# Performance work log

Measured on AMD Instinct MI355X. Metric: run time of the kernel, lower is better.

## Reference

```python
import jax, jax.numpy as jnp
import numpy as np

T, B, D, H, Q = 512, 256, 128, 256, 8


def _qgate(z, params):
    # Exact closed form of the PennyLane circuit:
    #   RX(z_w); RX(params_w) per wire; CNOT chain + wraparound CNOT(n-1,0); <Z_0>
    # => <Z_0> = prod_{w=1..Q-1} cos(z_w + params_w)   (wire 0 cancels out)
    theta = z + params  # (B, Q)
    return jnp.prod(jnp.cos(theta[:, 1:]), axis=1, keepdims=True)  # (B, 1)


def setup_inputs() -> dict:
    key = jax.random.key(0)
    ks = jax.random.split(key, 16)
    inputs = jax.random.normal(ks[0], (T, B, D), dtype=jnp.float32)
    hx0 = jnp.zeros((B, H), dtype=jnp.float32)
    cx0 = jnp.zeros((B, H), dtype=jnp.float32)
    s = 1.0 / np.sqrt(D + H)
    def lin(k1, k2):
        W = jax.random.uniform(k1, (Q, D + H), jnp.float32, -s, s)
        b = jax.random.uniform(k2, (Q,), jnp.float32, -s, s)
        return W, b
    Wf, bf = lin(ks[1], ks[2]); pf = jax.random.normal(ks[3], (Q,), jnp.float32)
    Wi, bi = lin(ks[4], ks[5]); pi = jax.random.normal(ks[6], (Q,), jnp.float32)
    Wu, bu = lin(ks[7], ks[8]); pu = jax.random.normal(ks[9], (Q,), jnp.float32)
    Wo, bo = lin(ks[10], ks[11]); po = jax.random.normal(ks[12], (Q,), jnp.float32)
    return {"inputs": inputs, "hx0": hx0, "cx0": cx0,
            "Wf": Wf, "bf": bf, "pf": pf,
            "Wi": Wi, "bi": bi, "pi": pi,
            "Wu": Wu, "bu": bu, "pu": pu,
            "Wo": Wo, "bo": bo, "po": po}


def reference(inputs, hx0, cx0, Wf, bf, pf, Wi, bi, pi, Wu, bu, pu, Wo, bo, po):
    def step(carry, x):
        hx, cx = carry
        comb = jnp.concatenate([x, hx], axis=1)  # (B, D+H)
        f = jax.nn.sigmoid(_qgate(comb @ Wf.T + bf, pf))  # (B,1)
        i = jax.nn.sigmoid(_qgate(comb @ Wi.T + bi, pi))
        g = jnp.tanh(_qgate(comb @ Wu.T + bu, pu))
        o = jax.nn.sigmoid(_qgate(comb @ Wo.T + bo, po))
        cx = f * cx + i * g
        hx = o * jnp.tanh(cx)
        return (hx, cx), hx

    (hx, cx), outputs = jax.lax.scan(step, (hx0, cx0), inputs)
    return outputs, (hx, cx)
```

## Files before the change

### kernel.cpp

```cpp
#include <hip/hip_runtime.h>
#include <cstdint>

#define T 512
#define B 256
#define D 128
#define H 256
#define DH 384
#define INV2PI 0.15915494309189535f
#define NLOG2E 1.442695041f

typedef float f32x4 __attribute__((ext_vector_type(4)));

#define WHS_OFF 0
#define HXS_OFF 64
#define CXF_OFF 131136
#define ZX_OFF  132096
#define ZX_FLOATS (T * B * 32)

__global__ __launch_bounds__(256) void k0_whs(const float* __restrict__ Wf, const float* __restrict__ Wi,
                                              const float* __restrict__ Wu, const float* __restrict__ Wo,
                                              float* __restrict__ whs) {
  int tid = threadIdx.x;
  int g = tid >> 6, r = tid & 63, q = r >> 3, part = r & 7;
  const float* W = (g == 0) ? Wf : (g == 1) ? Wi : (g == 2) ? Wu : Wo;
  const float* p = W + q * DH + D + part * 32;
  float s = 0.f;
#pragma unroll
  for (int h = 0; h < 32; ++h) s += p[h];
  s += __shfl_xor(s, 1);
  s += __shfl_xor(s, 2);
  s += __shfl_xor(s, 4);
  if (part == 0) whs[g * 8 + q] = s * INV2PI;
}

__global__ __launch_bounds__(128) void k1_gemm(const float* __restrict__ x,
    const float* __restrict__ Wf, const float* __restrict__ bf, const float* __restrict__ pf,
    const float* __restrict__ Wi, const float* __restrict__ bi, const float* __restrict__ pi,
    const float* __restrict__ Wu, const float* __restrict__ bu, const float* __restrict__ pu,
    const float* __restrict__ Wo, const float* __restrict__ bo, const float* __restrict__ po,
    float* __restrict__ zx) {
  __shared__ float wl[28 * 128];
  __shared__ float offs[32];
  int tid = threadIdx.x;
  const float* Ws[4] = {Wf, Wi, Wu, Wo};
  const float* bs[4] = {bf, bi, bu, bo};
  const float* ps[4] = {pf, pi, pu, po};
#pragma unroll
  for (int g = 0; g < 4; ++g)
    for (int i = tid; i < 896; i += 128) {
      int q = i >> 7, d = i & 127;
      wl[g * 896 + i] = Ws[g][(q + 1) * DH + d] * INV2PI;
    }
  if (tid < 32) {
    int g = tid >> 3, q = tid & 7;
    offs[tid] = (bs[g][q] + ps[g][q]) * INV2PI;
  }
  __syncthreads();

  int row0 = blockIdx.x * 512 + tid;
  const float4* x4 = (const float4*)x;
  const float4* wl4 = (const float4*)wl;

  float acc0[28], acc1[28], acc2[28], acc3[28];
#pragma unroll
  for (int r = 0; r < 28; ++r) acc0[r] = acc1[r] = acc2[r] = acc3[r] = 0.f;

  for (int k = 0; k < 32; ++k) {
    float4 xv0 = x4[(size_t)row0 * 32 + k];
    float4 xv1 = x4[(size_t)row0 * 32 + 4096 + k];
    float4 xv2 = x4[(size_t)row0 * 32 + 8192 + k];
    float4 xv3 = x4[(size_t)row0 * 32 + 12288 + k];
#pragma unroll
    for (int r = 0; r < 28; ++r) {
      float4 wv = wl4[r * 32 + k];
      acc0[r] = fmaf(xv0.x, wv.x, fmaf(xv0.y, wv.y, fmaf(xv0.z, wv.z, fmaf(xv0.w, wv.w, acc0[r]))));
      acc1[r] = fmaf(xv1.x, wv.x, fmaf(xv1.y, wv.y, fmaf(xv1.z, wv.z, fmaf(xv1.w, wv.w, acc1[r]))));
      acc2[r] = fmaf(xv2.x, wv.x, fmaf(xv2.y, wv.y, fmaf(xv2.z, wv.z, fmaf(xv2.w, wv.w, acc2[r]))));
      acc3[r] = fmaf(xv3.x, wv.x, fmaf(xv3.y, wv.y, fmaf(xv3.z, wv.z, fmaf(xv3.w, wv.w, acc3[r]))));
    }
  }

#define WROW(ACC, M)                                                                     \
  {                                                                                      \
    float4* zo = (float4*)(zx + (size_t)(row0 + (M)*128) * 32);                          \
    _Pragma("unroll") for (int g = 0; g < 4; ++g) {                                      \
      zo[g * 2 + 0] = make_float4(0.f, ACC[g * 7 + 0] + offs[g * 8 + 1],                 \
                                  ACC[g * 7 + 1] + offs[g * 8 + 2],                      \
                                  ACC[g * 7 + 2] + offs[g * 8 + 3]);                     \
      zo[g * 2 + 1] = make_float4(ACC[g * 7 + 3] + offs[g * 8 + 4],                      \
                                  ACC[g * 7 + 4] + offs[g * 8 + 5],                      \
                                  ACC[g * 7 + 5] + offs[g * 8 + 6],                      \
                                  ACC[g * 7 + 6] + offs[g * 8 + 7]);                     \
    }                                                                                    \
  }
  WROW(acc0, 0) WROW(acc1, 1) WROW(acc2, 2) WROW(acc3, 3)
#undef WROW
}

__device__ __forceinline__ float qcos(float x) {
  return __builtin_amdgcn_cosf(__builtin_amdgcn_fractf(x));
}
#define QBCAST(v, CTRL) __int_as_float(__builtin_amdgcn_mov_dpp(__float_as_int(v), (CTRL), 0xF, 0xF, true))

__device__ __forceinline__ void gload16(const float* g, float* l, int tid) {
#if __has_builtin(__builtin_amdgcn_global_load_lds)
  __builtin_amdgcn_global_load_lds((const __attribute__((address_space(1))) unsigned int*)g,
                                   (__attribute__((address_space(3))) unsigned int*)l, 16, 0, 0);
#else
  *(f32x4*)(l + tid * 4) = *(const f32x4*)g;
#endif
}

__device__ __forceinline__ void stage_tile(const float* gbase, int t0, float* lbase, int tid) {
#pragma unroll
  for (int s = 0; s < 16; ++s) {
    const float* g = gbase + (size_t)(t0 + s) * 8192;
    gload16(g, lbase + s * 512, tid);
    gload16(g + 256, lbase + s * 512 + 256, tid);
  }
}

#define STEP(S, ZA, ZB, TGT, TOFF)                                         \
  {                                                                        \
    f32x4 z0 = ZA, z1 = ZB;                                                \
    ZA = *(const f32x4*)((TGT) + (TOFF));                                  \
    ZB = *(const f32x4*)((TGT) + (TOFF) + 4);                              \
    float c1 = qcos(fmaf(hx, w[0], z0[1]));                                \
    float c2 = qcos(fmaf(hx, w[1], z0[2]));                                \
    float c3 = qcos(fmaf(hx, w[2], z0[3]));                                \
    float c4 = qcos(fmaf(hx, w[3], z1[0]));                                \
    float c5 = qcos(fmaf(hx, w[4], z1[1]));                                \
    float c6 = qcos(fmaf(hx, w[5], z1[2]));                                \
    float c7 = qcos(fmaf(hx, w[6], z1[3]));                                \
    float d4 = c7 * mk2;                                                   \
    float pr = ((c1 * c2) * (c3 * c4)) * ((c5 * c6) * d4);                 \
    float e = exp2f(pr);                                                   \
    float sv = __builtin_amdgcn_rcpf(1.f + e);                             \
    float val = fmaf(sv, sa, sb);                                          \
    float fv = QBCAST(val, 0x00);                                          \
    float iv = QBCAST(val, 0x55);                                          \
    float gv = QBCAST(val, 0xAA);                                          \
    float ov = QBCAST(val, 0xFF);                                          \
    cx = fmaf(fv, cx, iv * gv);                                            \
    float e2 = exp2f(cx * -2.885390082f);                                  \
    float tc = fmaf(__builtin_amdgcn_rcpf(1.f + e2), 2.f, -1.f);           \
    hx = ov * tc;                                                          \
    h##S = hx;                                                             \
  }

__global__ __launch_bounds__(64) void k2_scan(const float* __restrict__ zx, const float* __restrict__ whs,
                                              const float* __restrict__ hx0, const float* __restrict__ cx0,
                                              float* __restrict__ hxs, float* __restrict__ cxf) {
  __shared__ float zbuf[2 * 16 * 16 * 32];
  int tid = threadIdx.x;
  int g = tid & 3;
  int c = tid >> 2;
  int b = blockIdx.x * 16 + c;

  float w[7];
#pragma unroll
  for (int j = 0; j < 7; ++j) w[j] = whs[g * 8 + 1 + j];
  bool isU = (g == 2);
  float mk2 = isU ? -2.885390082f : -NLOG2E;
  float sa = isU ? 2.f : 1.f;
  float sb = isU ? -1.f : 0.f;

  float hx = hx0[(size_t)b * H];
  float cx = cx0[(size_t)b * H];

  float* zb = &zbuf[0];
  float* lb = zb + tid * 8;
  const float* gbase = zx + (size_t)blockIdx.x * 512 + (size_t)tid * 4;

  stage_tile(gbase, 0, zb, tid);
  stage_tile(gbase, 16, zb + 8192, tid);
  asm volatile("s_waitcnt vmcnt(32)" ::: "memory");

  f32x4 pA = *(const f32x4*)(lb + 0);
  f32x4 pB = *(const f32x4*)(lb + 4);
  f32x4 qA = *(const f32x4*)(lb + 512);
  f32x4 qB = *(const f32x4*)(lb + 516);

  float h0, h1, h2, h3, h4, h5, h6, h7, h8, h9, h10, h11, h12, h13, h14, h15;

  for (int kt = 0; kt < 32; ++kt) {
    float* bp = lb + (kt & 1) * 8192;
    float* bq = lb + ((kt & 1) ^ 1) * 8192;

    STEP(0, pA, pB, bp, 2 * 512)
    STEP(1, qA, qB, bp, 3 * 512)
    STEP(2, pA, pB, bp, 4 * 512)
    STEP(3, qA, qB, bp, 5 * 512)
    STEP(4, pA, pB, bp, 6 * 512)
    STEP(5, qA, qB, bp, 7 * 512)
    STEP(6, pA, pB, bp, 8 * 512)
    STEP(7, qA, qB, bp, 9 * 512)
    STEP(8, pA, pB, bp, 10 * 512)
    STEP(9, qA, qB, bp, 11 * 512)
    STEP(10, pA, pB, bp, 12 * 512)
    STEP(11, qA, qB, bp, 13 * 512)
    STEP(12, pA, pB, bp, 14 * 512)
    STEP(13, qA, qB, bp, 15 * 512)
    asm volatile("s_waitcnt vmcnt(0)" ::: "memory");
    STEP(14, pA, pB, bq, 0 * 512)
    STEP(15, qA, qB, bq, 1 * 512)

    if (g == 0) {
      float* hp = hxs + (size_t)(kt * 16) * B + b;
      hp[0 * B] = h0;   hp[1 * B] = h1;   hp[2 * B] = h2;   hp[3 * B] = h3;
      hp[4 * B] = h4;   hp[5 * B] = h5;   hp[6 * B] = h6;   hp[7 * B] = h7;
      hp[8 * B] = h8;   hp[9 * B] = h9;   hp[10 * B] = h10; hp[11 * B] = h11;
      hp[12 * B] = h12; hp[13 * B] = h13; hp[14 * B] = h14; hp[15 * B] = h15;
    }

    if (kt + 2 < 32) {
      asm volatile("s_waitcnt lgkmcnt(0)" ::: "memory");
      stage_tile(gbase, (kt + 2) * 16, zb + (kt & 1) * 8192, tid);
    }
  }
  if (g == 0) cxf[b] = cx;
}

__global__ __launch_bounds__(256) void k3_bcast(const float* __restrict__ hxs, const float* __restrict__ cxf,
                                                float* __restrict__ out) {
  const int TBH4 = (T * B * H) / 4;
  const int BH4 = (B * H) / 4;
  const int N4 = TBH4 + 2 * BH4;
  f32x4* out4 = (f32x4*)out;
  int stride = gridDim.x * blockDim.x;
  for (int i = blockIdx.x * blockDim.x + threadIdx.x; i < N4; i += stride) {
    float v;
    if (i < TBH4)            v = hxs[i >> 6];
    else if (i < TBH4 + BH4) v = hxs[(T - 1) * B + ((i - TBH4) >> 6)];
    else                     v = cxf[(i - TBH4 - BH4) >> 6];
    f32x4 pv = {v, v, v, v};
    __builtin_nontemporal_store(pv, &out4[i]);
  }
}

extern "C" void kernel_launch(void* const* d_in, const int* in_sizes, int n_in,
                              void* d_out, int out_size, void* d_ws, size_t ws_size,
                              hipStream_t stream) {
  const float* x   = (const float*)d_in[0];
  const float* hx0 = (const float*)d_in[1];
  const float* cx0 = (const float*)d_in[2];
  const float* Wf = (const float*)d_in[3];  const float* bf = (const float*)d_in[4];  const float* pf = (const float*)d_in[5];
  const float* Wi = (const float*)d_in[6];  const float* bi = (const float*)d_in[7];  const float* pi = (const float*)d_in[8];
  const float* Wu = (const float*)d_in[9];  const float* bu = (const float*)d_in[10]; const float* pu = (const float*)d_in[11];
  const float* Wo = (const float*)d_in[12]; const float* bo = (const float*)d_in[13]; const float* po = (const float*)d_in[14];

  float* wsf = (float*)d_ws;
  float* whs = wsf + WHS_OFF;
  float* hxs = wsf + HXS_OFF;
  float* cxf = wsf + CXF_OFF;
  float* out = (float*)d_out;
  float* zx = (ws_size >= (size_t)(ZX_OFF + ZX_FLOATS) * sizeof(float))
                  ? (wsf + ZX_OFF)
                  : (out + ((size_t)out_size - ZX_FLOATS));

  hipLaunchKernelGGL(k0_whs, dim3(1), dim3(256), 0, stream, Wf, Wi, Wu, Wo, whs);
  hipLaunchKernelGGL(k1_gemm, dim3(256), dim3(128), 0, stream,
                     x, Wf, bf, pf, Wi, bi, pi, Wu, bu, pu, Wo, bo, po, zx);
  hipLaunchKernelGGL(k2_scan, dim3(16), dim3(64), 0, stream, zx, whs, hx0, cx0, hxs, cxf);
  hipLaunchKernelGGL(k3_bcast, dim3(4096), dim3(256), 0, stream, hxs, cxf, out);
}
```

Measured before the change: 348.0 us.

## Replace LDS-staged scan with register double-buffered global loads and Padé tanh

```diff
diff --git a/kernel.cpp b/kernel.cpp
--- a/kernel.cpp
+++ b/kernel.cpp
@@ -7,7 +7,6 @@
 #define H 256
 #define DH 384
 #define INV2PI 0.15915494309189535f
-#define NLOG2E 1.442695041f
 
 typedef float f32x4 __attribute__((ext_vector_type(4)));
 
@@ -101,123 +100,103 @@
   return __builtin_amdgcn_cosf(__builtin_amdgcn_fractf(x));
 }
 #define QBCAST(v, CTRL) __int_as_float(__builtin_amdgcn_mov_dpp(__float_as_int(v), (CTRL), 0xF, 0xF, true))
-
-__device__ __forceinline__ void gload16(const float* g, float* l, int tid) {
-#if __has_builtin(__builtin_amdgcn_global_load_lds)
-  __builtin_amdgcn_global_load_lds((const __attribute__((address_space(1))) unsigned int*)g,
-                                   (__attribute__((address_space(3))) unsigned int*)l, 16, 0, 0);
-#else
-  *(f32x4*)(l + tid * 4) = *(const f32x4*)g;
-#endif
-}
-
-__device__ __forceinline__ void stage_tile(const float* gbase, int t0, float* lbase, int tid) {
-#pragma unroll
-  for (int s = 0; s < 16; ++s) {
-    const float* g = gbase + (size_t)(t0 + s) * 8192;
-    gload16(g, lbase + s * 512, tid);
-    gload16(g + 256, lbase + s * 512 + 256, tid);
-  }
-}
-
-#define STEP(S, ZA, ZB, TGT, TOFF)                                         \
+#define ASMBAR asm volatile("" ::: "memory")
+
+#define STEP(S, Z0, Z1)                                                    \
   {                                                                        \
-    f32x4 z0 = ZA, z1 = ZB;                                                \
-    ZA = *(const f32x4*)((TGT) + (TOFF));                                  \
-    ZB = *(const f32x4*)((TGT) + (TOFF) + 4);                              \
-    float c1 = qcos(fmaf(hx, w[0], z0[1]));                                \
-    float c2 = qcos(fmaf(hx, w[1], z0[2]));                                \
-    float c3 = qcos(fmaf(hx, w[2], z0[3]));                                \
-    float c4 = qcos(fmaf(hx, w[3], z1[0]));                                \
-    float c5 = qcos(fmaf(hx, w[4], z1[1]));                                \
-    float c6 = qcos(fmaf(hx, w[5], z1[2]));                                \
-    float c7 = qcos(fmaf(hx, w[6], z1[3]));                                \
-    float d4 = c7 * mk2;                                                   \
-    float pr = ((c1 * c2) * (c3 * c4)) * ((c5 * c6) * d4);                 \
-    float e = exp2f(pr);                                                   \
-    float sv = __builtin_amdgcn_rcpf(1.f + e);                             \
-    float val = fmaf(sv, sa, sb);                                          \
+    float c1 = qcos(fmaf(hx, w0, Z0[1]));                                  \
+    float c2 = qcos(fmaf(hx, w1, Z0[2]));                                  \
+    float c3 = qcos(fmaf(hx, w2, Z0[3]));                                  \
+    float c4 = qcos(fmaf(hx, w3, Z1[0]));                                  \
+    float c5 = qcos(fmaf(hx, w4, Z1[1]));                                  \
+    float c6 = qcos(fmaf(hx, w5, Z1[2]));                                  \
+    float c7 = qcos(fmaf(hx, w6, Z1[3])) * sgate;                          \
+    float y = ((c1 * c2) * (c3 * c4)) * ((c5 * c6) * c7);                  \
+    float t = y * y;                                                       \
+    float nn = fmaf(t, 105.f + t, 945.f);                                  \
+    float dd = fmaf(t, fmaf(15.f, t, 420.f), 945.f);                       \
+    float th = (y * nn) * __builtin_amdgcn_rcpf(dd);                       \
+    float val = fmaf(th, sgate, gb);                                       \
     float fv = QBCAST(val, 0x00);                                          \
     float iv = QBCAST(val, 0x55);                                          \
     float gv = QBCAST(val, 0xAA);                                          \
     float ov = QBCAST(val, 0xFF);                                          \
     cx = fmaf(fv, cx, iv * gv);                                            \
-    float e2 = exp2f(cx * -2.885390082f);                                  \
-    float tc = fmaf(__builtin_amdgcn_rcpf(1.f + e2), 2.f, -1.f);           \
-    hx = ov * tc;                                                          \
+    float t2 = cx * cx;                                                    \
+    float n2 = fmaf(t2, 105.f + t2, 945.f);                                \
+    float d2 = fmaf(t2, fmaf(15.f, t2, 420.f), 945.f);                     \
+    hx = ov * ((cx * n2) * __builtin_amdgcn_rcpf(d2));                     \
     h##S = hx;                                                             \
+  }
+
+#define LOADG(AP, BP, KT)                                                  \
+  {                                                                        \
+    const f32x4* gp = zp + (size_t)(KT) * 16384;                           \
+    AP##0 = gp[0];     BP##0 = gp[1];                                      \
+    AP##1 = gp[2048];  BP##1 = gp[2049];                                   \
+    AP##2 = gp[4096];  BP##2 = gp[4097];                                   \
+    AP##3 = gp[6144];  BP##3 = gp[6145];                                   \
+    AP##4 = gp[8192];  BP##4 = gp[8193];                                   \
+    AP##5 = gp[10240]; BP##5 = gp[10241];                                  \
+    AP##6 = gp[12288]; BP##6 = gp[12289];                                  \
+    AP##7 = gp[14336]; BP##7 = gp[14337];                                  \
+  }                                                                        \
+  ASMBAR;
+
+#define STEPS(AP, BP)                                                      \
+  STEP(0, AP##0, BP##0) STEP(1, AP##1, BP##1) STEP(2, AP##2, BP##2)        \
+  STEP(3, AP##3, BP##3) STEP(4, AP##4, BP##4) STEP(5, AP##5, BP##5)        \
+  STEP(6, AP##6, BP##6) STEP(7, AP##7, BP##7)
+
+#define STOREH(KT)                                                         \
+  if (g == 0) {                                                            \
+    float* hp = hxs + (size_t)(KT) * 8 * B + b;                            \
+    hp[0 * B] = h0; hp[1 * B] = h1; hp[2 * B] = h2; hp[3 * B] = h3;        \
+    hp[4 * B] = h4; hp[5 * B] = h5; hp[6 * B] = h6; hp[7 * B] = h7;        \
   }
 
 __global__ __launch_bounds__(64) void k2_scan(const float* __restrict__ zx, const float* __restrict__ whs,
                                               const float* __restrict__ hx0, const float* __restrict__ cx0,
                                               float* __restrict__ hxs, float* __restrict__ cxf) {
-  __shared__ float zbuf[2 * 16 * 16 * 32];
   int tid = threadIdx.x;
   int g = tid & 3;
-  int c = tid >> 2;
-  int b = blockIdx.x * 16 + c;
-
-  float w[7];
-#pragma unroll
-  for (int j = 0; j < 7; ++j) w[j] = whs[g * 8 + 1 + j];
+  int b = blockIdx.x * 16 + (tid >> 2);
+
+  float w0 = whs[g * 8 + 1], w1 = whs[g * 8 + 2], w2 = whs[g * 8 + 3], w3 = whs[g * 8 + 4];
+  float w4 = whs[g * 8 + 5], w5 = whs[g * 8 + 6], w6 = whs[g * 8 + 7];
   bool isU = (g == 2);
-  float mk2 = isU ? -2.885390082f : -NLOG2E;
-  float sa = isU ? 2.f : 1.f;
-  float sb = isU ? -1.f : 0.f;
+  float sgate = isU ? 1.f : 0.5f;
+  float gb = isU ? 0.f : 0.5f;
 
   float hx = hx0[(size_t)b * H];
   float cx = cx0[(size_t)b * H];
 
-  float* zb = &zbuf[0];
-  float* lb = zb + tid * 8;
-  const float* gbase = zx + (size_t)blockIdx.x * 512 + (size_t)tid * 4;
-
-  stage_tile(gbase, 0, zb, tid);
-  stage_tile(gbase, 16, zb + 8192, tid);
-  asm volatile("s_waitcnt vmcnt(32)" ::: "memory");
-
-  f32x4 pA = *(const f32x4*)(lb + 0);
-  f32x4 pB = *(const f32x4*)(lb + 4);
-  f32x4 qA = *(const f32x4*)(lb + 512);
-  f32x4 qB = *(const f32x4*)(lb + 516);
-
-  float h0, h1, h2, h3, h4, h5, h6, h7, h8, h9, h10, h11, h12, h13, h14, h15;
-
-  for (int kt = 0; kt < 32; ++kt) {
-    float* bp = lb + (kt & 1) * 8192;
-    float* bq = lb + ((kt & 1) ^ 1) * 8192;
-
-    STEP(0, pA, pB, bp, 2 * 512)
-    STEP(1, qA, qB, bp, 3 * 512)
-    STEP(2, pA, pB, bp, 4 * 512)
-    STEP(3, qA, qB, bp, 5 * 512)
-    STEP(4, pA, pB, bp, 6 * 512)
-    STEP(5, qA, qB, bp, 7 * 512)
-    STEP(6, pA, pB, bp, 8 * 512)
-    STEP(7, qA, qB, bp, 9 * 512)
-    STEP(8, pA, pB, bp, 10 * 512)
-    STEP(9, qA, qB, bp, 11 * 512)
-    STEP(10, pA, pB, bp, 12 * 512)
-    STEP(11, qA, qB, bp, 13 * 512)
-    STEP(12, pA, pB, bp, 14 * 512)
-    STEP(13, qA, qB, bp, 15 * 512)
-    asm volatile("s_waitcnt vmcnt(0)" ::: "memory");
-    STEP(14, pA, pB, bq, 0 * 512)
-    STEP(15, qA, qB, bq, 1 * 512)
-
-    if (g == 0) {
-      float* hp = hxs + (size_t)(kt * 16) * B + b;
-      hp[0 * B] = h0;   hp[1 * B] = h1;   hp[2 * B] = h2;   hp[3 * B] = h3;
-      hp[4 * B] = h4;   hp[5 * B] = h5;   hp[6 * B] = h6;   hp[7 * B] = h7;
-      hp[8 * B] = h8;   hp[9 * B] = h9;   hp[10 * B] = h10; hp[11 * B] = h11;
-      hp[12 * B] = h12; hp[13 * B] = h13; hp[14 * B] = h14; hp[15 * B] = h15;
-    }
-
-    if (kt + 2 < 32) {
-      asm volatile("s_waitcnt lgkmcnt(0)" ::: "memory");
-      stage_tile(gbase, (kt + 2) * 16, zb + (kt & 1) * 8192, tid);
-    }
-  }
+  const f32x4* zp = (const f32x4*)zx + ((size_t)b * 8 + (size_t)g * 2);
+
+  f32x4 aA0, aA1, aA2, aA3, aA4, aA5, aA6, aA7, aB0, aB1, aB2, aB3, aB4, aB5, aB6, aB7;
+  f32x4 bA0, bA1, bA2, bA3, bA4, bA5, bA6, bA7, bB0, bB1, bB2, bB3, bB4, bB5, bB6, bB7;
+  float h0, h1, h2, h3, h4, h5, h6, h7;
+
+  LOADG(aA, aB, 0)
+  LOADG(bA, bB, 1)
+  asm volatile("s_waitcnt vmcnt(16)" ::: "memory");
+  STEPS(aA, aB)
+  STOREH(0)
+
+  for (int kt = 1; kt < 63; kt += 2) {
+    asm volatile("s_waitcnt vmcnt(8)" ::: "memory");
+    LOADG(aA, aB, kt + 1)
+    STEPS(bA, bB)
+    STOREH(kt)
+    asm volatile("s_waitcnt vmcnt(8)" ::: "memory");
+    LOADG(bA, bB, kt + 2)
+    STEPS(aA, aB)
+    STOREH(kt + 1)
+  }
+  asm volatile("s_waitcnt vmcnt(8)" ::: "memory");
+  STEPS(bA, bB)
+  STOREH(63)
+
   if (g == 0) cxf[b] = cx;
 }
 
```

Result: slower. 374.5 us (+7.6%).
